# Performance work log

Hardware: AMD Instinct MI355X
Metric: run time of the kernel (lower is better)

Reference implementation:

```python
import jax, jax.numpy as jnp
import numpy as np

IN_CH = 32
OUT_CH = 32
B, N = 1, 100000
E = 1600000
BN_EPS = 1e-5


def setup_inputs() -> dict:
    key = jax.random.key(0)
    k1, k2, k3 = jax.random.split(key, 3)
    x = jax.random.normal(k1, (B, IN_CH, N, 1), dtype=jnp.float32)
    edge_index = jax.random.randint(k2, (2, E), 0, B * N, dtype=jnp.int64)
    # Conv1d(in*2 -> out, kernel_size=1, bias=False): weight [out, 2*in]
    W = jax.random.normal(k3, (OUT_CH, 2 * IN_CH), dtype=jnp.float32) * (1.0 / np.sqrt(2 * IN_CH))
    gamma = jnp.ones((OUT_CH,), dtype=jnp.float32)
    beta = jnp.zeros((OUT_CH,), dtype=jnp.float32)
    return {"x": x, "edge_index": edge_index, "W": W, "gamma": gamma, "beta": beta}


def reference(x, edge_index, W, gamma, beta):
    Bb, C, Nn, _ = x.shape
    out_ch = W.shape[0]
    # faithful to torch: x.squeeze(-1).view(B*N, C) (raw row-major reshape)
    x_flat = x[..., 0].reshape(Bb * Nn, C)
    src, tgt = edge_index[0], edge_index[1]
    x_s = x_flat[src]                      # [E, C] gather
    x_t = x_flat[tgt]                      # [E, C] gather
    ef = jnp.concatenate([x_s, x_t - x_s], axis=1)  # [E, 2C]
    y = ef @ W.T                           # 1x1 conv == GEMM, [E, out]
    # BatchNorm1d in training mode: batch stats over edge dim (biased var)
    mean = jnp.mean(y, axis=0)
    var = jnp.mean(jnp.square(y - mean), axis=0)
    y = (y - mean) * jax.lax.rsqrt(var + BN_EPS) * gamma + beta
    # ELU (alpha=1)
    y = jnp.where(y > 0, y, jnp.expm1(y))
    out = jnp.zeros((Bb * Nn, out_ch), dtype=y.dtype).at[src].add(y)  # scatter-add
    return out.reshape(Bb, out_ch, Nn)[..., None]
```

## Files before the change

kernel.cpp:

```cpp
#include <hip/hip_runtime.h>
#include <hip/hip_bf16.h>
#include <math.h>

#define NCH 32

typedef unsigned short ushort_t;
typedef unsigned int uint_t;
typedef unsigned char uchar_t;

static __device__ __forceinline__ float bf2f(ushort_t b) {
    return __uint_as_float(((uint_t)b) << 16);
}
static __device__ __forceinline__ ushort_t f2bf(float f) {
    __hip_bfloat16 h = __float2bfloat16(f);
    return *reinterpret_cast<ushort_t*>(&h);
}

using f32x2 = __attribute__((ext_vector_type(2))) float;

template <typename T>
__device__ __forceinline__ auto pkAddImpl(T* p, T v, int)
    -> decltype(unsafeAtomicAdd(p, v), void()) {
    unsafeAtomicAdd(p, v);
}
template <typename T>
__device__ void pkAddImpl(T* p, T v, long) {
    uint_t* q = reinterpret_cast<uint_t*>(p);
    uint_t vv = *reinterpret_cast<uint_t*>(&v);
    uint_t cur = *q;
    while (true) {
        float lo = bf2f((ushort_t)(cur & 0xFFFF)) + bf2f((ushort_t)(vv & 0xFFFF));
        float hi = bf2f((ushort_t)(cur >> 16)) + bf2f((ushort_t)(vv >> 16));
        uint_t nw = (uint_t)f2bf(lo) | ((uint_t)f2bf(hi) << 16);
        uint_t prev = atomicCAS(q, cur, nw);
        if (prev == cur) break;
        cur = prev;
    }
}
static __device__ __forceinline__ void pkAdd(__hip_bfloat162* p, float z0, float z1) {
    __hip_bfloat162 v;
    v.x = __float2bfloat16(z0);
    v.y = __float2bfloat16(z1);
    pkAddImpl(p, v, 0);
}


__global__ __launch_bounds__(256) void k_uv3(
    const float* __restrict__ x, const float* __restrict__ W,
    ushort_t* __restrict__ uh, ushort_t* __restrict__ vh,
    uchar_t* __restrict__ uq, uchar_t* __restrict__ vq, int N)
{
    __shared__ float At[NCH * NCH];
    __shared__ float Bt[NCH * NCH];
    for (int i = threadIdx.x; i < NCH * NCH; i += 256) {
        const int k = i >> 5, c = i & 31;
        const float w1 = W[c * 64 + k];
        const float w2 = W[c * 64 + 32 + k];
        At[i] = w1 - w2;
        Bt[i] = w2;
    }
    __syncthreads();

    const int n = blockIdx.x * 8 + (threadIdx.x >> 5);
    const int c = threadIdx.x & 31;
    if (n >= N) return;

    const float xc = x[(size_t)n * NCH + c];
    float su = 0.f, sv = 0.f;
#pragma unroll
    for (int k = 0; k < NCH; ++k) {
        const float xk = __shfl(xc, k, 32);
        su = fmaf(At[k * 32 + c], xk, su);
        sv = fmaf(Bt[k * 32 + c], xk, sv);
    }
    uh[(size_t)n * NCH + c] = f2bf(su);
    vh[(size_t)n * NCH + c] = f2bf(sv);
    uq[(size_t)n * NCH + c] =
        (uchar_t)(__builtin_amdgcn_cvt_pk_fp8_f32(su, su, 0, false) & 0xFF);
    vq[(size_t)n * NCH + c] =
        (uchar_t)(__builtin_amdgcn_cvt_pk_fp8_f32(sv, sv, 0, false) & 0xFF);
}

__global__ __launch_bounds__(256) void k_stats8(
    const uchar_t* __restrict__ uq, const uchar_t* __restrict__ vq,
    const int* __restrict__ srci, const int* __restrict__ tgti,
    float* __restrict__ partials, int E)
{
    const ushort_t* __restrict__ uq16 = (const ushort_t*)uq;
    const ushort_t* __restrict__ vq16 = (const ushort_t*)vq;
    const int l  = threadIdx.x & 15;
    const int g  = (blockIdx.x * 256 + threadIdx.x) >> 4;
    const int nG = (gridDim.x * 256) >> 4;

    float s0 = 0.f, s1 = 0.f, q0 = 0.f, q1 = 0.f;
    int e = g;
    for (; e + 3 * nG < E; e += 4 * nG) {
        const int ea = e, eb = e + nG, ec = e + 2 * nG, ed = e + 3 * nG;
        const int sa = srci[ea], sb = srci[eb], sc = srci[ec], sd = srci[ed];
        const int ta = tgti[ea], tb = tgti[eb], tc = tgti[ec], td = tgti[ed];
        const ushort_t ua = uq16[(size_t)sa * 16 + l];
        const ushort_t ub = uq16[(size_t)sb * 16 + l];
        const ushort_t uc = uq16[(size_t)sc * 16 + l];
        const ushort_t ud = uq16[(size_t)sd * 16 + l];
        const ushort_t va = vq16[(size_t)ta * 16 + l];
        const ushort_t vb = vq16[(size_t)tb * 16 + l];
        const ushort_t vc = vq16[(size_t)tc * 16 + l];
        const ushort_t vd = vq16[(size_t)td * 16 + l];
#pragma unroll
        for (int k = 0; k < 4; ++k) {
            const ushort_t uu = (k == 0) ? ua : (k == 1) ? ub : (k == 2) ? uc : ud;
            const ushort_t vv = (k == 0) ? va : (k == 1) ? vb : (k == 2) ? vc : vd;
            const f32x2 uf = __builtin_amdgcn_cvt_pk_f32_fp8((int)uu, false);
            const f32x2 vf = __builtin_amdgcn_cvt_pk_f32_fp8((int)vv, false);
            const float y0 = uf.x + vf.x;
            const float y1 = uf.y + vf.y;
            s0 += y0; q0 = fmaf(y0, y0, q0);
            s1 += y1; q1 = fmaf(y1, y1, q1);
        }
    }
    for (; e < E; e += nG) {
        const int s = srci[e], t = tgti[e];
        const f32x2 uf = __builtin_amdgcn_cvt_pk_f32_fp8((int)uq16[(size_t)s * 16 + l], false);
        const f32x2 vf = __builtin_amdgcn_cvt_pk_f32_fp8((int)vq16[(size_t)t * 16 + l], false);
        const float y0 = uf.x + vf.x;
        const float y1 = uf.y + vf.y;
        s0 += y0; q0 = fmaf(y0, y0, q0);
        s1 += y1; q1 = fmaf(y1, y1, q1);
    }

    __shared__ float sL[16][32];
    __shared__ float qL[16][32];
    const int grp = threadIdx.x >> 4;
    sL[grp][2 * l + 0] = s0;
    sL[grp][2 * l + 1] = s1;
    qL[grp][2 * l + 0] = q0;
    qL[grp][2 * l + 1] = q1;
    __syncthreads();
    if (threadIdx.x < 32) {
        float a = 0.f;
#pragma unroll
        for (int r = 0; r < 16; ++r) a += sL[r][threadIdx.x];
        partials[(size_t)blockIdx.x * 64 + threadIdx.x] = a;
    } else if (threadIdx.x < 64) {
        const int cc = threadIdx.x - 32;
        float a = 0.f;
#pragma unroll
        for (int r = 0; r < 16; ++r) a += qL[r][cc];
        partials[(size_t)blockIdx.x * 64 + 32 + cc] = a;
    }
}

__global__ __launch_bounds__(256) void k_finalize(
    const float* __restrict__ partials, int nblocks,
    const float* __restrict__ gamma, const float* __restrict__ beta,
    float* __restrict__ ab, float invE)
{
    __shared__ float acc[4][64];
    const int vtx = threadIdx.x & 63, chunk = threadIdx.x >> 6;
    float s = 0.f;
    for (int r = chunk; r < nblocks; r += 4) s += partials[(size_t)r * 64 + vtx];
    acc[chunk][vtx] = s;
    __syncthreads();
    if (threadIdx.x < 64) acc[0][vtx] = acc[0][vtx] + acc[1][vtx] + acc[2][vtx] + acc[3][vtx];
    __syncthreads();
    if (threadIdx.x < 32) {
        const int c = threadIdx.x;
        float mean = acc[0][c] * invE;
        float var  = acc[0][32 + c] * invE - mean * mean;
        float rstd = rsqrtf(var + 1e-5f);
        float a = gamma[c] * rstd;
        ab[c] = a; ab[32 + c] = beta[c] - mean * a;
    }
}

__global__ __launch_bounds__(256) void k_apply_pk(
    const ushort_t* __restrict__ uh, const ushort_t* __restrict__ vh,
    const int* __restrict__ srci, const int* __restrict__ tgti,
    const float* __restrict__ ab,
    __hip_bfloat162* __restrict__ outh, int E)
{
    const uint_t* __restrict__ uh32 = (const uint_t*)uh;
    const uint_t* __restrict__ vh32 = (const uint_t*)vh;
    const int l  = threadIdx.x & 15;
    const float a0 = ab[2 * l + 0], a1 = ab[2 * l + 1];
    const float b0 = ab[32 + 2 * l + 0], b1 = ab[32 + 2 * l + 1];
    const int g  = (blockIdx.x * 256 + threadIdx.x) >> 4;
    const int nG = (gridDim.x * 256) >> 4;

    int e = g;
    for (; e + 3 * nG < E; e += 4 * nG) {
        const int ea = e, eb = e + nG, ec = e + 2 * nG, ed = e + 3 * nG;
        const int sa = srci[ea], sb = srci[eb], sc = srci[ec], sd = srci[ed];
        const int ta = tgti[ea], tb = tgti[eb], tc = tgti[ec], td = tgti[ed];
        const uint_t Ua = uh32[(size_t)sa * 16 + l];
        const uint_t Ub = uh32[(size_t)sb * 16 + l];
        const uint_t Uc = uh32[(size_t)sc * 16 + l];
        const uint_t Ud = uh32[(size_t)sd * 16 + l];
        const uint_t Va = vh32[(size_t)ta * 16 + l];
        const uint_t Vb = vh32[(size_t)tb * 16 + l];
        const uint_t Vc = vh32[(size_t)tc * 16 + l];
        const uint_t Vd = vh32[(size_t)td * 16 + l];
        const int ss[4] = {sa, sb, sc, sd};
        const uint_t UU[4] = {Ua, Ub, Uc, Ud};
        const uint_t VV[4] = {Va, Vb, Vc, Vd};
#pragma unroll
        for (int k = 0; k < 4; ++k) {
            const float y0 = bf2f((ushort_t)(UU[k] & 0xFFFF)) + bf2f((ushort_t)(VV[k] & 0xFFFF));
            const float y1 = bf2f((ushort_t)(UU[k] >> 16))    + bf2f((ushort_t)(VV[k] >> 16));
            float z0 = fmaf(a0, y0, b0);
            float z1 = fmaf(a1, y1, b1);
            z0 = (z0 > 0.f) ? z0 : (__expf(z0) - 1.0f);
            z1 = (z1 > 0.f) ? z1 : (__expf(z1) - 1.0f);
            pkAdd(&outh[(size_t)ss[k] * 16 + l], z0, z1);
        }
    }
    for (; e < E; e += nG) {
        const int s = srci[e], t = tgti[e];
        const uint_t U = uh32[(size_t)s * 16 + l];
        const uint_t V = vh32[(size_t)t * 16 + l];
        const float y0 = bf2f((ushort_t)(U & 0xFFFF)) + bf2f((ushort_t)(V & 0xFFFF));
        const float y1 = bf2f((ushort_t)(U >> 16))    + bf2f((ushort_t)(V >> 16));
        float z0 = fmaf(a0, y0, b0);
        float z1 = fmaf(a1, y1, b1);
        z0 = (z0 > 0.f) ? z0 : (__expf(z0) - 1.0f);
        z1 = (z1 > 0.f) ? z1 : (__expf(z1) - 1.0f);
        pkAdd(&outh[(size_t)s * 16 + l], z0, z1);
    }
}

__global__ __launch_bounds__(256) void k_cvt(
    const uint_t* __restrict__ outh32, float* __restrict__ out, int M)
{
    const int i = blockIdx.x * 256 + threadIdx.x;
    if (i >= M) return;
    const uint_t w = outh32[i];
    float2 f;
    f.x = bf2f((ushort_t)(w & 0xFFFF));
    f.y = bf2f((ushort_t)(w >> 16));
    ((float2*)out)[i] = f;
}

__global__ __launch_bounds__(256) void k_stats_hist(
    const float* __restrict__ x,
    const int* __restrict__ srci, const int* __restrict__ tgti,
    const float* __restrict__ W,
    float* __restrict__ partials, int E)
{
    float sum[NCH], ssq[NCH];
#pragma unroll
    for (int c = 0; c < NCH; ++c) { sum[c] = 0.f; ssq[c] = 0.f; }
    const int stride = gridDim.x * blockDim.x;
    for (int e = blockIdx.x * blockDim.x + threadIdx.x; e < E; e += stride) {
        const int s = srci[e], t = tgti[e];
        const float4* ps = (const float4*)(x + (size_t)s * NCH);
        const float4* pt = (const float4*)(x + (size_t)t * NCH);
        float xs[NCH], dx[NCH];
#pragma unroll
        for (int i = 0; i < 8; ++i) {
            float4 a = ps[i], bb = pt[i];
            xs[4*i+0] = a.x; xs[4*i+1] = a.y; xs[4*i+2] = a.z; xs[4*i+3] = a.w;
            dx[4*i+0] = bb.x - a.x; dx[4*i+1] = bb.y - a.y;
            dx[4*i+2] = bb.z - a.z; dx[4*i+3] = bb.w - a.w;
        }
#pragma unroll
        for (int c = 0; c < NCH; ++c) {
            const float* wr = W + c * 64;
            float y = 0.f;
#pragma unroll
            for (int k = 0; k < NCH; ++k) y = fmaf(wr[k], xs[k], y);
#pragma unroll
            for (int k = 0; k < NCH; ++k) y = fmaf(wr[32 + k], dx[k], y);
            sum[c] += y;
            ssq[c] = fmaf(y, y, ssq[c]);
        }
    }
#pragma unroll
    for (int c = 0; c < NCH; ++c) {
#pragma unroll
        for (int off = 32; off > 0; off >>= 1) {
            sum[c] += __shfl_down(sum[c], off);
            ssq[c] += __shfl_down(ssq[c], off);
        }
    }
    __shared__ float red[4][64];
    const int lane = threadIdx.x & 63, wave = threadIdx.x >> 6;
    if (lane == 0) {
#pragma unroll
        for (int c = 0; c < NCH; ++c) { red[wave][c] = sum[c]; red[wave][NCH+c] = ssq[c]; }
    }
    __syncthreads();
    if (threadIdx.x < 64)
        partials[(size_t)blockIdx.x * 64 + threadIdx.x] =
            red[0][threadIdx.x] + red[1][threadIdx.x] + red[2][threadIdx.x] + red[3][threadIdx.x];
}

__global__ __launch_bounds__(256) void k_apply_atomic(
    const float* __restrict__ x,
    const int* __restrict__ srci, const int* __restrict__ tgti,
    const float* __restrict__ W, const float* __restrict__ ab,
    float* __restrict__ out, int E)
{
    const int e = blockIdx.x * 256 + threadIdx.x;
    if (e >= E) return;
    const int s = srci[e], t = tgti[e];
    const float4* ps = (const float4*)(x + (size_t)s * NCH);
    const float4* pt = (const float4*)(x + (size_t)t * NCH);
    float xs[NCH], dx[NCH];
#pragma unroll
    for (int i = 0; i < 8; ++i) {
        float4 a = ps[i], bb = pt[i];
        xs[4*i+0] = a.x; xs[4*i+1] = a.y; xs[4*i+2] = a.z; xs[4*i+3] = a.w;
        dx[4*i+0] = bb.x - a.x; dx[4*i+1] = bb.y - a.y;
        dx[4*i+2] = bb.z - a.z; dx[4*i+3] = bb.w - a.w;
    }
    float* orow = out + (size_t)s * NCH;
#pragma unroll
    for (int c = 0; c < NCH; ++c) {
        const float* wr = W + c * 64;
        float y = 0.f;
#pragma unroll
        for (int k = 0; k < NCH; ++k) y = fmaf(wr[k], xs[k], y);
#pragma unroll
        for (int k = 0; k < NCH; ++k) y = fmaf(wr[32 + k], dx[k], y);
        float z = fmaf(ab[c], y, ab[32 + c]);
        z = (z > 0.f) ? z : (__expf(z) - 1.0f);
        atomicAdd(orow + c, z);
    }
}

extern "C" void kernel_launch(void* const* d_in, const int* in_sizes, int n_in,
                              void* d_out, int out_size, void* d_ws, size_t ws_size,
                              hipStream_t stream)
{
    const float* x     = (const float*)d_in[0];
    const int*   ei    = (const int*)d_in[1];
    const float* W     = (const float*)d_in[2];
    const float* gamma = (const float*)d_in[3];
    const float* beta  = (const float*)d_in[4];
    const int E = in_sizes[1] / 2;
    const int N = in_sizes[0] / NCH;
    const int* srci = ei;
    const int* tgti = ei + E;

    const int SB = 1024;
    const int AB = 2048;

    size_t need = (size_t)N * NCH * (2 + 2 + 1 + 1 + 2)
                + ((size_t)SB * 64 + 64) * 4;

    if (ws_size >= need) {
        ushort_t* uh      = (ushort_t*)d_ws;
        ushort_t* vh      = uh + (size_t)N * NCH;
        uchar_t*  uq      = (uchar_t*)(vh + (size_t)N * NCH);
        uchar_t*  vq      = uq + (size_t)N * NCH;
        __hip_bfloat162* outh = (__hip_bfloat162*)(vq + (size_t)N * NCH);
        float*    partials= (float*)((ushort_t*)outh + (size_t)N * NCH);
        float*    ab      = partials + (size_t)SB * 64;

        hipMemsetAsync(outh, 0, (size_t)N * NCH * 2, stream);
        k_uv3<<<(N + 7) / 8, 256, 0, stream>>>(x, W, uh, vh, uq, vq, N);
        k_stats8<<<SB, 256, 0, stream>>>(uq, vq, srci, tgti, partials, E);
        k_finalize<<<1, 256, 0, stream>>>(partials, SB, gamma, beta, ab, 1.0f / (float)E);
        k_apply_pk<<<AB, 256, 0, stream>>>(uh, vh, srci, tgti, ab, outh, E);
        k_cvt<<<(N * 16 + 255) / 256, 256, 0, stream>>>((const uint_t*)outh,
                                                        (float*)d_out, N * 16);
    } else {
        const int SBf = 512;
        float* ab       = (float*)d_ws;
        float* partials = ab + 64;
        hipMemsetAsync(d_out, 0, (size_t)out_size * sizeof(float), stream);
        k_stats_hist<<<SBf, 256, 0, stream>>>(x, srci, tgti, W, partials, E);
        k_finalize<<<1, 256, 0, stream>>>(partials, SBf, gamma, beta, ab, 1.0f / (float)E);
        k_apply_atomic<<<(E + 255) / 256, 256, 0, stream>>>(x, srci, tgti, W, ab,
                                                            (float*)d_out, E);
    }
}
```

Before: 309.3 us.

## Build CSR by source node and replace atomic scatter with per-node segmented reduction

Builds a per-call CSR of edges grouped by source: a degree histogram fused into the u/v projection kernel, a single-block prefix scan, and an atomic cursor scatter of targets. Stats and apply kernels then walk each node's neighbour list. The source-side u values are loaded once per node, and the output is accumulated in registers and written directly in fp32. This removes the bf16 packed atomic adds, the zero-fill of the bf16 output buffer, the conversion kernel and the fp8 u buffer. In exchange it adds three kernels, edge-level atomics for the histogram and scatter, and a serial single-block scan over 100k nodes that may be slow.

```diff
diff --git a/kernel.cpp b/kernel.cpp
--- a/kernel.cpp
+++ b/kernel.cpp
@@ -18,37 +18,12 @@
 
 using f32x2 = __attribute__((ext_vector_type(2))) float;
 
-template <typename T>
-__device__ __forceinline__ auto pkAddImpl(T* p, T v, int)
-    -> decltype(unsafeAtomicAdd(p, v), void()) {
-    unsafeAtomicAdd(p, v);
-}
-template <typename T>
-__device__ void pkAddImpl(T* p, T v, long) {
-    uint_t* q = reinterpret_cast<uint_t*>(p);
-    uint_t vv = *reinterpret_cast<uint_t*>(&v);
-    uint_t cur = *q;
-    while (true) {
-        float lo = bf2f((ushort_t)(cur & 0xFFFF)) + bf2f((ushort_t)(vv & 0xFFFF));
-        float hi = bf2f((ushort_t)(cur >> 16)) + bf2f((ushort_t)(vv >> 16));
-        uint_t nw = (uint_t)f2bf(lo) | ((uint_t)f2bf(hi) << 16);
-        uint_t prev = atomicCAS(q, cur, nw);
-        if (prev == cur) break;
-        cur = prev;
-    }
-}
-static __device__ __forceinline__ void pkAdd(__hip_bfloat162* p, float z0, float z1) {
-    __hip_bfloat162 v;
-    v.x = __float2bfloat16(z0);
-    v.y = __float2bfloat16(z1);
-    pkAddImpl(p, v, 0);
-}
-
-
-__global__ __launch_bounds__(256) void k_uv3(
+
+__global__ __launch_bounds__(256) void k_uv_hist(
     const float* __restrict__ x, const float* __restrict__ W,
     ushort_t* __restrict__ uh, ushort_t* __restrict__ vh,
-    uchar_t* __restrict__ uq, uchar_t* __restrict__ vq, int N)
+    uchar_t* __restrict__ vq,
+    const int* __restrict__ srci, int* __restrict__ deg, int N, int E)
 {
     __shared__ float At[NCH * NCH];
     __shared__ float Bt[NCH * NCH];
@@ -63,74 +38,121 @@
 
     const int n = blockIdx.x * 8 + (threadIdx.x >> 5);
     const int c = threadIdx.x & 31;
-    if (n >= N) return;
-
-    const float xc = x[(size_t)n * NCH + c];
-    float su = 0.f, sv = 0.f;
-#pragma unroll
-    for (int k = 0; k < NCH; ++k) {
-        const float xk = __shfl(xc, k, 32);
-        su = fmaf(At[k * 32 + c], xk, su);
-        sv = fmaf(Bt[k * 32 + c], xk, sv);
-    }
-    uh[(size_t)n * NCH + c] = f2bf(su);
-    vh[(size_t)n * NCH + c] = f2bf(sv);
-    uq[(size_t)n * NCH + c] =
-        (uchar_t)(__builtin_amdgcn_cvt_pk_fp8_f32(su, su, 0, false) & 0xFF);
-    vq[(size_t)n * NCH + c] =
-        (uchar_t)(__builtin_amdgcn_cvt_pk_fp8_f32(sv, sv, 0, false) & 0xFF);
-}
-
-__global__ __launch_bounds__(256) void k_stats8(
-    const uchar_t* __restrict__ uq, const uchar_t* __restrict__ vq,
+    if (n < N) {
+        const float xc = x[(size_t)n * NCH + c];
+        float su = 0.f, sv = 0.f;
+#pragma unroll
+        for (int k = 0; k < NCH; ++k) {
+            const float xk = __shfl(xc, k, 32);
+            su = fmaf(At[k * 32 + c], xk, su);
+            sv = fmaf(Bt[k * 32 + c], xk, sv);
+        }
+        uh[(size_t)n * NCH + c] = f2bf(su);
+        vh[(size_t)n * NCH + c] = f2bf(sv);
+        vq[(size_t)n * NCH + c] =
+            (uchar_t)(__builtin_amdgcn_cvt_pk_fp8_f32(sv, sv, 0, false) & 0xFF);
+    }
+
+    const int stride = gridDim.x * 256;
+    for (int e = blockIdx.x * 256 + threadIdx.x; e < E; e += stride)
+        atomicAdd(&deg[srci[e]], 1);
+}
+
+__global__ __launch_bounds__(1024) void k_scan(
+    const int* __restrict__ deg, int* __restrict__ row_start,
+    int* __restrict__ cursor, int N)
+{
+    __shared__ int wsum[16];
+    __shared__ int wpre[16];
+    const int t = threadIdx.x;
+    const int lane = t & 63, wid = t >> 6;
+    const int per = (N + 1023) >> 10;
+    const int b = t * per;
+    const int e = (b + per < N) ? (b + per) : N;
+
+    int s = 0;
+    for (int i = b; i < e; ++i) s += deg[i];
+
+    int v = s;
+#pragma unroll
+    for (int off = 1; off < 64; off <<= 1) {
+        int nv = __shfl_up(v, off, 64);
+        if (lane >= off) v += nv;
+    }
+    if (lane == 63) wsum[wid] = v;
+    __syncthreads();
+    if (t == 0) {
+        int acc = 0;
+#pragma unroll
+        for (int w = 0; w < 16; ++w) { wpre[w] = acc; acc += wsum[w]; }
+    }
+    __syncthreads();
+
+    int run = wpre[wid] + v - s;
+    for (int i = b; i < e; ++i) {
+        const int d = deg[i];
+        row_start[i] = run;
+        cursor[i] = run;
+        run += d;
+    }
+    if (t == 1023) row_start[N] = run;
+}
+
+__global__ __launch_bounds__(256) void k_scatter(
     const int* __restrict__ srci, const int* __restrict__ tgti,
-    float* __restrict__ partials, int E)
-{
-    const ushort_t* __restrict__ uq16 = (const ushort_t*)uq;
+    int* __restrict__ cursor, int* __restrict__ csr, int E)
+{
+    const int e = blockIdx.x * 256 + threadIdx.x;
+    if (e >= E) return;
+    const int s = srci[e], t = tgti[e];
+    const int pos = atomicAdd(&cursor[s], 1);
+    csr[pos] = t;
+}
+
+__global__ __launch_bounds__(256) void k_stats_csr(
+    const ushort_t* __restrict__ uh, const uchar_t* __restrict__ vq,
+    const int* __restrict__ row_start, const int* __restrict__ csr,
+    float* __restrict__ partials, int N)
+{
+    const uint_t* __restrict__ uh32 = (const uint_t*)uh;
     const ushort_t* __restrict__ vq16 = (const ushort_t*)vq;
-    const int l  = threadIdx.x & 15;
-    const int g  = (blockIdx.x * 256 + threadIdx.x) >> 4;
-    const int nG = (gridDim.x * 256) >> 4;
+    const int l   = threadIdx.x & 15;
+    const int grp = threadIdx.x >> 4;
+    const int G  = blockIdx.x * 16 + grp;
+    const int nG = gridDim.x * 16;
 
     float s0 = 0.f, s1 = 0.f, q0 = 0.f, q1 = 0.f;
-    int e = g;
-    for (; e + 3 * nG < E; e += 4 * nG) {
-        const int ea = e, eb = e + nG, ec = e + 2 * nG, ed = e + 3 * nG;
-        const int sa = srci[ea], sb = srci[eb], sc = srci[ec], sd = srci[ed];
-        const int ta = tgti[ea], tb = tgti[eb], tc = tgti[ec], td = tgti[ed];
-        const ushort_t ua = uq16[(size_t)sa * 16 + l];
-        const ushort_t ub = uq16[(size_t)sb * 16 + l];
-        const ushort_t uc = uq16[(size_t)sc * 16 + l];
-        const ushort_t ud = uq16[(size_t)sd * 16 + l];
-        const ushort_t va = vq16[(size_t)ta * 16 + l];
-        const ushort_t vb = vq16[(size_t)tb * 16 + l];
-        const ushort_t vc = vq16[(size_t)tc * 16 + l];
-        const ushort_t vd = vq16[(size_t)td * 16 + l];
-#pragma unroll
-        for (int k = 0; k < 4; ++k) {
-            const ushort_t uu = (k == 0) ? ua : (k == 1) ? ub : (k == 2) ? uc : ud;
-            const ushort_t vv = (k == 0) ? va : (k == 1) ? vb : (k == 2) ? vc : vd;
-            const f32x2 uf = __builtin_amdgcn_cvt_pk_f32_fp8((int)uu, false);
-            const f32x2 vf = __builtin_amdgcn_cvt_pk_f32_fp8((int)vv, false);
-            const float y0 = uf.x + vf.x;
-            const float y1 = uf.y + vf.y;
-            s0 += y0; q0 = fmaf(y0, y0, q0);
-            s1 += y1; q1 = fmaf(y1, y1, q1);
-        }
-    }
-    for (; e < E; e += nG) {
-        const int s = srci[e], t = tgti[e];
-        const f32x2 uf = __builtin_amdgcn_cvt_pk_f32_fp8((int)uq16[(size_t)s * 16 + l], false);
-        const f32x2 vf = __builtin_amdgcn_cvt_pk_f32_fp8((int)vq16[(size_t)t * 16 + l], false);
-        const float y0 = uf.x + vf.x;
-        const float y1 = uf.y + vf.y;
-        s0 += y0; q0 = fmaf(y0, y0, q0);
-        s1 += y1; q1 = fmaf(y1, y1, q1);
+    for (int n = G; n < N; n += nG) {
+        const int r0 = row_start[n], r1 = row_start[n + 1];
+        const uint_t U = uh32[(size_t)n * 16 + l];
+        const float u0 = bf2f((ushort_t)(U & 0xFFFF));
+        const float u1 = bf2f((ushort_t)(U >> 16));
+        float sv0 = 0.f, sv1 = 0.f, vv0 = 0.f, vv1 = 0.f;
+        int j = r0;
+        for (; j + 1 < r1; j += 2) {
+            const int ta = csr[j], tb = csr[j + 1];
+            const f32x2 va = __builtin_amdgcn_cvt_pk_f32_fp8((int)vq16[(size_t)ta * 16 + l], false);
+            const f32x2 vb = __builtin_amdgcn_cvt_pk_f32_fp8((int)vq16[(size_t)tb * 16 + l], false);
+            sv0 += va.x + vb.x;
+            sv1 += va.y + vb.y;
+            vv0 = fmaf(va.x, va.x, vv0); vv0 = fmaf(vb.x, vb.x, vv0);
+            vv1 = fmaf(va.y, va.y, vv1); vv1 = fmaf(vb.y, vb.y, vv1);
+        }
+        if (j < r1) {
+            const f32x2 va = __builtin_amdgcn_cvt_pk_f32_fp8((int)vq16[(size_t)csr[j] * 16 + l], false);
+            sv0 += va.x; sv1 += va.y;
+            vv0 = fmaf(va.x, va.x, vv0);
+            vv1 = fmaf(va.y, va.y, vv1);
+        }
+        const float d = (float)(r1 - r0);
+        s0 += fmaf(d, u0, sv0);
+        s1 += fmaf(d, u1, sv1);
+        q0 += fmaf(d, u0 * u0, fmaf(2.f * u0, sv0, vv0));
+        q1 += fmaf(d, u1 * u1, fmaf(2.f * u1, sv1, vv1));
     }
 
     __shared__ float sL[16][32];
     __shared__ float qL[16][32];
-    const int grp = threadIdx.x >> 4;
     sL[grp][2 * l + 0] = s0;
     sL[grp][2 * l + 1] = s1;
     qL[grp][2 * l + 0] = q0;
@@ -173,71 +195,59 @@
     }
 }
 
-__global__ __launch_bounds__(256) void k_apply_pk(
+__global__ __launch_bounds__(256) void k_apply_csr(
     const ushort_t* __restrict__ uh, const ushort_t* __restrict__ vh,
-    const int* __restrict__ srci, const int* __restrict__ tgti,
-    const float* __restrict__ ab,
-    __hip_bfloat162* __restrict__ outh, int E)
+    const int* __restrict__ row_start, const int* __restrict__ csr,
+    const float* __restrict__ ab, float* __restrict__ out, int N)
 {
     const uint_t* __restrict__ uh32 = (const uint_t*)uh;
     const uint_t* __restrict__ vh32 = (const uint_t*)vh;
-    const int l  = threadIdx.x & 15;
+    const int l   = threadIdx.x & 15;
+    const int grp = threadIdx.x >> 4;
     const float a0 = ab[2 * l + 0], a1 = ab[2 * l + 1];
     const float b0 = ab[32 + 2 * l + 0], b1 = ab[32 + 2 * l + 1];
-    const int g  = (blockIdx.x * 256 + threadIdx.x) >> 4;
-    const int nG = (gridDim.x * 256) >> 4;
-
-    int e = g;
-    for (; e + 3 * nG < E; e += 4 * nG) {
-        const int ea = e, eb = e + nG, ec = e + 2 * nG, ed = e + 3 * nG;
-        const int sa = srci[ea], sb = srci[eb], sc = srci[ec], sd = srci[ed];
-        const int ta = tgti[ea], tb = tgti[eb], tc = tgti[ec], td = tgti[ed];
-        const uint_t Ua = uh32[(size_t)sa * 16 + l];
-        const uint_t Ub = uh32[(size_t)sb * 16 + l];
-        const uint_t Uc = uh32[(size_t)sc * 16 + l];
-        const uint_t Ud = uh32[(size_t)sd * 16 + l];
-        const uint_t Va = vh32[(size_t)ta * 16 + l];
-        const uint_t Vb = vh32[(size_t)tb * 16 + l];
-        const uint_t Vc = vh32[(size_t)tc * 16 + l];
-        const uint_t Vd = vh32[(size_t)td * 16 + l];
-        const int ss[4] = {sa, sb, sc, sd};
-        const uint_t UU[4] = {Ua, Ub, Uc, Ud};
-        const uint_t VV[4] = {Va, Vb, Vc, Vd};
-#pragma unroll
-        for (int k = 0; k < 4; ++k) {
-            const float y0 = bf2f((ushort_t)(UU[k] & 0xFFFF)) + bf2f((ushort_t)(VV[k] & 0xFFFF));
-            const float y1 = bf2f((ushort_t)(UU[k] >> 16))    + bf2f((ushort_t)(VV[k] >> 16));
+    const int G  = blockIdx.x * 16 + grp;
+    const int nG = gridDim.x * 16;
+
+    for (int n = G; n < N; n += nG) {
+        const int r0 = row_start[n], r1 = row_start[n + 1];
+        const uint_t U = uh32[(size_t)n * 16 + l];
+        const float u0 = bf2f((ushort_t)(U & 0xFFFF));
+        const float u1 = bf2f((ushort_t)(U >> 16));
+        float acc0 = 0.f, acc1 = 0.f;
+        int j = r0;
+        for (; j + 1 < r1; j += 2) {
+            const int ta = csr[j], tb = csr[j + 1];
+            const uint_t Va = vh32[(size_t)ta * 16 + l];
+            const uint_t Vb = vh32[(size_t)tb * 16 + l];
+            float y0 = u0 + bf2f((ushort_t)(Va & 0xFFFF));
+            float y1 = u1 + bf2f((ushort_t)(Va >> 16));
             float z0 = fmaf(a0, y0, b0);
             float z1 = fmaf(a1, y1, b1);
             z0 = (z0 > 0.f) ? z0 : (__expf(z0) - 1.0f);
             z1 = (z1 > 0.f) ? z1 : (__expf(z1) - 1.0f);
-            pkAdd(&outh[(size_t)ss[k] * 16 + l], z0, z1);
-        }
-    }
-    for (; e < E; e += nG) {
-        const int s = srci[e], t = tgti[e];
-        const uint_t U = uh32[(size_t)s * 16 + l];
-        const uint_t V = vh32[(size_t)t * 16 + l];
-        const float y0 = bf2f((ushort_t)(U & 0xFFFF)) + bf2f((ushort_t)(V & 0xFFFF));
-        const float y1 = bf2f((ushort_t)(U >> 16))    + bf2f((ushort_t)(V >> 16));
-        float z0 = fmaf(a0, y0, b0);
-        float z1 = fmaf(a1, y1, b1);
-        z0 = (z0 > 0.f) ? z0 : (__expf(z0) - 1.0f);
-        z1 = (z1 > 0.f) ? z1 : (__expf(z1) - 1.0f);
-        pkAdd(&outh[(size_t)s * 16 + l], z0, z1);
-    }
-}
-
-__global__ __launch_bounds__(256) void k_cvt(
-    const uint_t* __restrict__ outh32, float* __restrict__ out, int M)
-{
-    const int i = blockIdx.x * 256 + threadIdx.x;
-    if (i >= M) return;
-    const uint_t w = outh32[i];
-    float2 f;
-    f.x = bf2f((ushort_t)(w & 0xFFFF));
-    f.y = bf2f((ushort_t)(w >> 16));
-    ((float2*)out)[i] = f;
+            acc0 += z0; acc1 += z1;
+            y0 = u0 + bf2f((ushort_t)(Vb & 0xFFFF));
+            y1 = u1 + bf2f((ushort_t)(Vb >> 16));
+            z0 = fmaf(a0, y0, b0);
+            z1 = fmaf(a1, y1, b1);
+            z0 = (z0 > 0.f) ? z0 : (__expf(z0) - 1.0f);
+            z1 = (z1 > 0.f) ? z1 : (__expf(z1) - 1.0f);
+            acc0 += z0; acc1 += z1;
+        }
+        if (j < r1) {
+            const uint_t Va = vh32[(size_t)csr[j] * 16 + l];
+            float y0 = u0 + bf2f((ushort_t)(Va & 0xFFFF));
+            float y1 = u1 + bf2f((ushort_t)(Va >> 16));
+            float z0 = fmaf(a0, y0, b0);
+            float z1 = fmaf(a1, y1, b1);
+            z0 = (z0 > 0.f) ? z0 : (__expf(z0) - 1.0f);
+            z1 = (z1 > 0.f) ? z1 : (__expf(z1) - 1.0f);
+            acc0 += z0; acc1 += z1;
+        }
+        float2 o; o.x = acc0; o.y = acc1;
+        ((float2*)out)[(size_t)n * 16 + l] = o;
+    }
 }
 
 __global__ __launch_bounds__(256) void k_stats_hist(
@@ -345,33 +355,33 @@
     const int SB = 1024;
     const int AB = 2048;
 
-    size_t need = (size_t)N * NCH * (2 + 2 + 1 + 1 + 2)
-                + ((size_t)SB * 64 + 64) * 4;
+    ushort_t* uh      = (ushort_t*)d_ws;
+    ushort_t* vh      = uh + (size_t)N * NCH;
+    uchar_t*  vq      = (uchar_t*)(vh + (size_t)N * NCH);
+    int*      deg     = (int*)(vq + (size_t)N * NCH);
+    int*      row_start = deg + N;
+    int*      cursor  = row_start + (N + 1);
+    int*      csr     = cursor + N;
+    float*    partials = (float*)(csr + E);
+    float*    ab      = partials + (size_t)SB * 64;
+    const size_t need = (size_t)((char*)(ab + 64) - (char*)d_ws);
 
     if (ws_size >= need) {
-        ushort_t* uh      = (ushort_t*)d_ws;
-        ushort_t* vh      = uh + (size_t)N * NCH;
-        uchar_t*  uq      = (uchar_t*)(vh + (size_t)N * NCH);
-        uchar_t*  vq      = uq + (size_t)N * NCH;
-        __hip_bfloat162* outh = (__hip_bfloat162*)(vq + (size_t)N * NCH);
-        float*    partials= (float*)((ushort_t*)outh + (size_t)N * NCH);
-        float*    ab      = partials + (size_t)SB * 64;
-
-        hipMemsetAsync(outh, 0, (size_t)N * NCH * 2, stream);
-        k_uv3<<<(N + 7) / 8, 256, 0, stream>>>(x, W, uh, vh, uq, vq, N);
-        k_stats8<<<SB, 256, 0, stream>>>(uq, vq, srci, tgti, partials, E);
+        hipMemsetAsync(deg, 0, (size_t)N * sizeof(int), stream);
+        k_uv_hist<<<(N + 7) / 8, 256, 0, stream>>>(x, W, uh, vh, vq, srci, deg, N, E);
+        k_scan<<<1, 1024, 0, stream>>>(deg, row_start, cursor, N);
+        k_scatter<<<(E + 255) / 256, 256, 0, stream>>>(srci, tgti, cursor, csr, E);
+        k_stats_csr<<<SB, 256, 0, stream>>>(uh, vq, row_start, csr, partials, N);
         k_finalize<<<1, 256, 0, stream>>>(partials, SB, gamma, beta, ab, 1.0f / (float)E);
-        k_apply_pk<<<AB, 256, 0, stream>>>(uh, vh, srci, tgti, ab, outh, E);
-        k_cvt<<<(N * 16 + 255) / 256, 256, 0, stream>>>((const uint_t*)outh,
-                                                        (float*)d_out, N * 16);
+        k_apply_csr<<<AB, 256, 0, stream>>>(uh, vh, row_start, csr, ab, (float*)d_out, N);
     } else {
         const int SBf = 512;
-        float* ab       = (float*)d_ws;
-        float* partials = ab + 64;
+        float* abf      = (float*)d_ws;
+        float* partialsf = abf + 64;
         hipMemsetAsync(d_out, 0, (size_t)out_size * sizeof(float), stream);
-        k_stats_hist<<<SBf, 256, 0, stream>>>(x, srci, tgti, W, partials, E);
-        k_finalize<<<1, 256, 0, stream>>>(partials, SBf, gamma, beta, ab, 1.0f / (float)E);
-        k_apply_atomic<<<(E + 255) / 256, 256, 0, stream>>>(x, srci, tgti, W, ab,
+        k_stats_hist<<<SBf, 256, 0, stream>>>(x, srci, tgti, W, partialsf, E);
+        k_finalize<<<1, 256, 0, stream>>>(partialsf, SBf, gamma, beta, abf, 1.0f / (float)E);
+        k_apply_atomic<<<(E + 255) / 256, 256, 0, stream>>>(x, srci, tgti, W, abf,
                                                             (float*)d_out, E);
     }
 }
```

New measurement: 657.2 us. +112.5%, slower.

## Fuse all stages into one cooperative persistent kernel with grid syncs

Applied to the files above, without the earlier changes.

Replaces the memset plus five separate launches with a single cooperative kernel sized to full occupancy. The kernel runs the projection, zeroing, stats, finalize, scatter-apply and conversion phases, with grid.sync between them. This targets launch overhead and inter-kernel gaps. In exchange the grid is capped at occupancy-limited block counts, and the serial finalize on block 0 plus the grid barriers add sync costs.

```diff
diff --git a/kernel.cpp b/kernel.cpp
--- a/kernel.cpp
+++ b/kernel.cpp
@@ -1,8 +1,11 @@
 #include <hip/hip_runtime.h>
 #include <hip/hip_bf16.h>
+#include <hip/hip_cooperative_groups.h>
 #include <math.h>
 
 #define NCH 32
+
+namespace cg = cooperative_groups;
 
 typedef unsigned short ushort_t;
 typedef unsigned int uint_t;
@@ -45,6 +48,214 @@
 }
 
 
+__global__ __launch_bounds__(256) void k_fused(
+    const float* __restrict__ x, const int* __restrict__ srci,
+    const int* __restrict__ tgti, const float* __restrict__ W,
+    const float* __restrict__ gamma, const float* __restrict__ beta,
+    ushort_t* __restrict__ uh, ushort_t* __restrict__ vh,
+    uchar_t* __restrict__ uq, uchar_t* __restrict__ vq,
+    __hip_bfloat162* __restrict__ outh, float* __restrict__ partials,
+    float* __restrict__ ab, float* __restrict__ out, int N, int E)
+{
+    cg::grid_group grid = cg::this_grid();
+
+    __shared__ float At[NCH * NCH];
+    __shared__ float Bt[NCH * NCH];
+    __shared__ float sL[16][32];
+    __shared__ float qL[16][32];
+    __shared__ float acc[4][64];
+
+    for (int i = threadIdx.x; i < NCH * NCH; i += 256) {
+        const int k = i >> 5, c = i & 31;
+        const float w1 = W[c * 64 + k];
+        const float w2 = W[c * 64 + 32 + k];
+        At[i] = w1 - w2;
+        Bt[i] = w2;
+    }
+    __syncthreads();
+    {
+        const int sub = threadIdx.x >> 5;
+        const int c = threadIdx.x & 31;
+        for (int n0 = blockIdx.x * 8; n0 < N; n0 += gridDim.x * 8) {
+            const int n = n0 + sub;
+            if (n < N) {
+                const float xc = x[(size_t)n * NCH + c];
+                float su = 0.f, sv = 0.f;
+#pragma unroll
+                for (int k = 0; k < NCH; ++k) {
+                    const float xk = __shfl(xc, k, 32);
+                    su = fmaf(At[k * 32 + c], xk, su);
+                    sv = fmaf(Bt[k * 32 + c], xk, sv);
+                }
+                uh[(size_t)n * NCH + c] = f2bf(su);
+                vh[(size_t)n * NCH + c] = f2bf(sv);
+                uq[(size_t)n * NCH + c] =
+                    (uchar_t)(__builtin_amdgcn_cvt_pk_fp8_f32(su, su, 0, false) & 0xFF);
+                vq[(size_t)n * NCH + c] =
+                    (uchar_t)(__builtin_amdgcn_cvt_pk_fp8_f32(sv, sv, 0, false) & 0xFF);
+            }
+        }
+        uint_t* o32 = (uint_t*)outh;
+        const int M = N * 16;
+        for (int i = blockIdx.x * 256 + threadIdx.x; i < M; i += gridDim.x * 256)
+            o32[i] = 0u;
+    }
+    __threadfence();
+    grid.sync();
+
+    {
+        const ushort_t* __restrict__ uq16 = (const ushort_t*)uq;
+        const ushort_t* __restrict__ vq16 = (const ushort_t*)vq;
+        const int l  = threadIdx.x & 15;
+        const int g  = (blockIdx.x * 256 + threadIdx.x) >> 4;
+        const int nG = (gridDim.x * 256) >> 4;
+
+        float s0 = 0.f, s1 = 0.f, q0 = 0.f, q1 = 0.f;
+        int e = g;
+        for (; e + 3 * nG < E; e += 4 * nG) {
+            const int ea = e, eb = e + nG, ec = e + 2 * nG, ed = e + 3 * nG;
+            const int sa = srci[ea], sb = srci[eb], sc = srci[ec], sd = srci[ed];
+            const int ta = tgti[ea], tb = tgti[eb], tc = tgti[ec], td = tgti[ed];
+            const ushort_t ua = uq16[(size_t)sa * 16 + l];
+            const ushort_t ub = uq16[(size_t)sb * 16 + l];
+            const ushort_t uc = uq16[(size_t)sc * 16 + l];
+            const ushort_t ud = uq16[(size_t)sd * 16 + l];
+            const ushort_t va = vq16[(size_t)ta * 16 + l];
+            const ushort_t vb = vq16[(size_t)tb * 16 + l];
+            const ushort_t vc = vq16[(size_t)tc * 16 + l];
+            const ushort_t vd = vq16[(size_t)td * 16 + l];
+#pragma unroll
+            for (int k = 0; k < 4; ++k) {
+                const ushort_t uu = (k == 0) ? ua : (k == 1) ? ub : (k == 2) ? uc : ud;
+                const ushort_t vvv = (k == 0) ? va : (k == 1) ? vb : (k == 2) ? vc : vd;
+                const f32x2 uf = __builtin_amdgcn_cvt_pk_f32_fp8((int)uu, false);
+                const f32x2 vf = __builtin_amdgcn_cvt_pk_f32_fp8((int)vvv, false);
+                const float y0 = uf.x + vf.x;
+                const float y1 = uf.y + vf.y;
+                s0 += y0; q0 = fmaf(y0, y0, q0);
+                s1 += y1; q1 = fmaf(y1, y1, q1);
+            }
+        }
+        for (; e < E; e += nG) {
+            const int s = srci[e], t = tgti[e];
+            const f32x2 uf = __builtin_amdgcn_cvt_pk_f32_fp8((int)uq16[(size_t)s * 16 + l], false);
+            const f32x2 vf = __builtin_amdgcn_cvt_pk_f32_fp8((int)vq16[(size_t)t * 16 + l], false);
+            const float y0 = uf.x + vf.x;
+            const float y1 = uf.y + vf.y;
+            s0 += y0; q0 = fmaf(y0, y0, q0);
+            s1 += y1; q1 = fmaf(y1, y1, q1);
+        }
+
+        const int grp = threadIdx.x >> 4;
+        sL[grp][2 * l + 0] = s0;
+        sL[grp][2 * l + 1] = s1;
+        qL[grp][2 * l + 0] = q0;
+        qL[grp][2 * l + 1] = q1;
+        __syncthreads();
+        if (threadIdx.x < 32) {
+            float a = 0.f;
+#pragma unroll
+            for (int r = 0; r < 16; ++r) a += sL[r][threadIdx.x];
+            partials[(size_t)blockIdx.x * 64 + threadIdx.x] = a;
+        } else if (threadIdx.x < 64) {
+            const int cc = threadIdx.x - 32;
+            float a = 0.f;
+#pragma unroll
+            for (int r = 0; r < 16; ++r) a += qL[r][cc];
+            partials[(size_t)blockIdx.x * 64 + 32 + cc] = a;
+        }
+    }
+    __threadfence();
+    grid.sync();
+
+    if (blockIdx.x == 0) {
+        const int vtx = threadIdx.x & 63, chunk = threadIdx.x >> 6;
+        float s = 0.f;
+        for (int r = chunk; r < (int)gridDim.x; r += 4)
+            s += partials[(size_t)r * 64 + vtx];
+        acc[chunk][vtx] = s;
+        __syncthreads();
+        if (threadIdx.x < 64)
+            acc[0][vtx] = acc[0][vtx] + acc[1][vtx] + acc[2][vtx] + acc[3][vtx];
+        __syncthreads();
+        if (threadIdx.x < 32) {
+            const int c = threadIdx.x;
+            const float invE = 1.0f / (float)E;
+            float mean = acc[0][c] * invE;
+            float var  = acc[0][32 + c] * invE - mean * mean;
+            float rstd = rsqrtf(var + 1e-5f);
+            float a = gamma[c] * rstd;
+            ab[c] = a; ab[32 + c] = beta[c] - mean * a;
+        }
+    }
+    __threadfence();
+    grid.sync();
+
+    {
+        const uint_t* __restrict__ uh32 = (const uint_t*)uh;
+        const uint_t* __restrict__ vh32 = (const uint_t*)vh;
+        const int l  = threadIdx.x & 15;
+        const float a0 = ab[2 * l + 0], a1 = ab[2 * l + 1];
+        const float b0 = ab[32 + 2 * l + 0], b1 = ab[32 + 2 * l + 1];
+        const int g  = (blockIdx.x * 256 + threadIdx.x) >> 4;
+        const int nG = (gridDim.x * 256) >> 4;
+
+        int e = g;
+        for (; e + 3 * nG < E; e += 4 * nG) {
+            const int ea = e, eb = e + nG, ec = e + 2 * nG, ed = e + 3 * nG;
+            const int sa = srci[ea], sb = srci[eb], sc = srci[ec], sd = srci[ed];
+            const int ta = tgti[ea], tb = tgti[eb], tc = tgti[ec], td = tgti[ed];
+            const uint_t Ua = uh32[(size_t)sa * 16 + l];
+            const uint_t Ub = uh32[(size_t)sb * 16 + l];
+            const uint_t Uc = uh32[(size_t)sc * 16 + l];
+            const uint_t Ud = uh32[(size_t)sd * 16 + l];
+            const uint_t Va = vh32[(size_t)ta * 16 + l];
+            const uint_t Vb = vh32[(size_t)tb * 16 + l];
+            const uint_t Vc = vh32[(size_t)tc * 16 + l];
+            const uint_t Vd = vh32[(size_t)td * 16 + l];
+            const int ss[4] = {sa, sb, sc, sd};
+            const uint_t UU[4] = {Ua, Ub, Uc, Ud};
+            const uint_t VV[4] = {Va, Vb, Vc, Vd};
+#pragma unroll
+            for (int k = 0; k < 4; ++k) {
+                const float y0 = bf2f((ushort_t)(UU[k] & 0xFFFF)) + bf2f((ushort_t)(VV[k] & 0xFFFF));
+                const float y1 = bf2f((ushort_t)(UU[k] >> 16))    + bf2f((ushort_t)(VV[k] >> 16));
+                float z0 = fmaf(a0, y0, b0);
+                float z1 = fmaf(a1, y1, b1);
+                z0 = (z0 > 0.f) ? z0 : (__expf(z0) - 1.0f);
+                z1 = (z1 > 0.f) ? z1 : (__expf(z1) - 1.0f);
+                pkAdd(&outh[(size_t)ss[k] * 16 + l], z0, z1);
+            }
+        }
+        for (; e < E; e += nG) {
+            const int s = srci[e], t = tgti[e];
+            const uint_t U = uh32[(size_t)s * 16 + l];
+            const uint_t V = vh32[(size_t)t * 16 + l];
+            const float y0 = bf2f((ushort_t)(U & 0xFFFF)) + bf2f((ushort_t)(V & 0xFFFF));
+            const float y1 = bf2f((ushort_t)(U >> 16))    + bf2f((ushort_t)(V >> 16));
+            float z0 = fmaf(a0, y0, b0);
+            float z1 = fmaf(a1, y1, b1);
+            z0 = (z0 > 0.f) ? z0 : (__expf(z0) - 1.0f);
+            z1 = (z1 > 0.f) ? z1 : (__expf(z1) - 1.0f);
+            pkAdd(&outh[(size_t)s * 16 + l], z0, z1);
+        }
+    }
+    __threadfence();
+    grid.sync();
+
+    {
+        const uint_t* o32 = (const uint_t*)outh;
+        const int M = N * 16;
+        for (int i = blockIdx.x * 256 + threadIdx.x; i < M; i += gridDim.x * 256) {
+            const uint_t w = o32[i];
+            float2 f;
+            f.x = bf2f((ushort_t)(w & 0xFFFF));
+            f.y = bf2f((ushort_t)(w >> 16));
+            ((float2*)out)[i] = f;
+        }
+    }
+}
+
 __global__ __launch_bounds__(256) void k_uv3(
     const float* __restrict__ x, const float* __restrict__ W,
     ushort_t* __restrict__ uh, ushort_t* __restrict__ vh,
@@ -60,11 +271,9 @@
         Bt[i] = w2;
     }
     __syncthreads();
-
     const int n = blockIdx.x * 8 + (threadIdx.x >> 5);
     const int c = threadIdx.x & 31;
     if (n >= N) return;
-
     const float xc = x[(size_t)n * NCH + c];
     float su = 0.f, sv = 0.f;
 #pragma unroll
@@ -342,21 +551,55 @@
     const int* srci = ei;
     const int* tgti = ei + E;
 
-    const int SB = 1024;
-    const int AB = 2048;
-
-    size_t need = (size_t)N * NCH * (2 + 2 + 1 + 1 + 2)
-                + ((size_t)SB * 64 + 64) * 4;
+    static int coopBlocks = -2;
+    if (coopBlocks == -2) {
+        int nb = 0;
+        hipError_t e1 = hipOccupancyMaxActiveBlocksPerMultiprocessor(&nb, k_fused, 256, 0);
+        int nCU = 256;
+        hipDeviceProp_t prop;
+        int dev = 0;
+        if (hipGetDevice(&dev) == hipSuccess &&
+            hipGetDeviceProperties(&prop, dev) == hipSuccess &&
+            prop.multiProcessorCount > 0)
+            nCU = prop.multiProcessorCount;
+        if (e1 != hipSuccess || nb < 1) coopBlocks = 0;
+        else {
+            long long g = (long long)nb * nCU;
+            coopBlocks = (int)((g > 2048) ? 2048 : g);
+            if (coopBlocks < 64) coopBlocks = 0;
+        }
+    }
+
+    const int GB = (coopBlocks > 0) ? coopBlocks : 2048;
+
+    ushort_t* uh      = (ushort_t*)d_ws;
+    ushort_t* vh      = uh + (size_t)N * NCH;
+    uchar_t*  uq      = (uchar_t*)(vh + (size_t)N * NCH);
+    uchar_t*  vq      = uq + (size_t)N * NCH;
+    __hip_bfloat162* outh = (__hip_bfloat162*)(vq + (size_t)N * NCH);
+    float*    partials= (float*)((ushort_t*)outh + (size_t)N * NCH);
+    float*    ab      = partials + (size_t)2048 * 64;
+    const size_t need = (size_t)((char*)(ab + 64) - (char*)d_ws);
+
+    if (ws_size >= need && coopBlocks > 0) {
+        int Nv = N, Ev = E;
+        void* args[] = {
+            (void*)&x, (void*)&srci, (void*)&tgti, (void*)&W,
+            (void*)&gamma, (void*)&beta,
+            (void*)&uh, (void*)&vh, (void*)&uq, (void*)&vq,
+            (void*)&outh, (void*)&partials, (void*)&ab,
+            (void*)&d_out, (void*)&Nv, (void*)&Ev
+        };
+        hipError_t err = hipLaunchCooperativeKernel(
+            (const void*)k_fused, dim3(coopBlocks), dim3(256), args, 0, stream);
+        if (err == hipSuccess) return;
+        coopBlocks = 0;
+        (void)GB;
+    }
 
     if (ws_size >= need) {
-        ushort_t* uh      = (ushort_t*)d_ws;
-        ushort_t* vh      = uh + (size_t)N * NCH;
-        uchar_t*  uq      = (uchar_t*)(vh + (size_t)N * NCH);
-        uchar_t*  vq      = uq + (size_t)N * NCH;
-        __hip_bfloat162* outh = (__hip_bfloat162*)(vq + (size_t)N * NCH);
-        float*    partials= (float*)((ushort_t*)outh + (size_t)N * NCH);
-        float*    ab      = partials + (size_t)SB * 64;
-
+        const int SB = 1024;
+        const int AB = 2048;
         hipMemsetAsync(outh, 0, (size_t)N * NCH * 2, stream);
         k_uv3<<<(N + 7) / 8, 256, 0, stream>>>(x, W, uh, vh, uq, vq, N);
         k_stats8<<<SB, 256, 0, stream>>>(uq, vq, srci, tgti, partials, E);
@@ -366,12 +609,12 @@
                                                         (float*)d_out, N * 16);
     } else {
         const int SBf = 512;
-        float* ab       = (float*)d_ws;
-        float* partials = ab + 64;
+        float* abf      = (float*)d_ws;
+        float* partialsf = abf + 64;
         hipMemsetAsync(d_out, 0, (size_t)out_size * sizeof(float), stream);
-        k_stats_hist<<<SBf, 256, 0, stream>>>(x, srci, tgti, W, partials, E);
-        k_finalize<<<1, 256, 0, stream>>>(partials, SBf, gamma, beta, ab, 1.0f / (float)E);
-        k_apply_atomic<<<(E + 255) / 256, 256, 0, stream>>>(x, srci, tgti, W, ab,
+        k_stats_hist<<<SBf, 256, 0, stream>>>(x, srci, tgti, W, partialsf, E);
+        k_finalize<<<1, 256, 0, stream>>>(partialsf, SBf, gamma, beta, abf, 1.0f / (float)E);
+        k_apply_atomic<<<(E + 255) / 256, 256, 0, stream>>>(x, srci, tgti, W, abf,
                                                             (float*)d_out, E);
     }
 }
```

New measurement: 1.085 ms. 251% more time.
